# Kernel tuning notes

Measured on AMD Instinct MI355X. Metric: run time of the kernel, lower is better.

## Reference

```python
import jax, jax.numpy as jnp
import numpy as np

N = 50000
E = 800000
IN_C, HID_C, OUT_C = 64, 96, 32


def setup_inputs() -> dict:
    key = jax.random.key(0)
    ks = jax.random.split(key, 8)
    x = jax.random.normal(ks[0], (N, IN_C), dtype=jnp.float32)
    edge_index = jax.random.randint(ks[1], (2, E), 0, N, dtype=jnp.int32)
    W1 = jax.random.normal(ks[2], (IN_C, HID_C), dtype=jnp.float32) / np.sqrt(IN_C)
    b1 = jnp.zeros((HID_C,), jnp.float32)
    W2 = jax.random.normal(ks[3], (HID_C, HID_C), dtype=jnp.float32) / np.sqrt(HID_C)
    b2 = jnp.zeros((HID_C,), jnp.float32)
    Wfc = jax.random.normal(ks[4], (HID_C, OUT_C), dtype=jnp.float32) / np.sqrt(HID_C)
    bfc = jnp.zeros((OUT_C,), jnp.float32)
    return {"x": x, "edge_index": edge_index, "W1": W1, "b1": b1,
            "W2": W2, "b2": b2, "Wfc": Wfc, "bfc": bfc}


def _gcn_conv(x, src, dst, norm, W, b):
    # x' = D^{-1/2}(A+I)D^{-1/2} (x W) + b   (PyG GCNConv default)
    h = x @ W                                # [N, C_out]
    msg = h[src] * norm[:, None]             # gather + edge scaling
    agg = jax.ops.segment_sum(msg, dst, num_segments=N)  # scatter-add
    return agg + b


def reference(x, edge_index, W1, b1, W2, b2, Wfc, bfc):
    loop = jnp.arange(N, dtype=edge_index.dtype)
    src = jnp.concatenate([edge_index[0], loop])  # add self-loops
    dst = jnp.concatenate([edge_index[1], loop])
    deg = jax.ops.segment_sum(jnp.ones(src.shape[0], jnp.float32), dst,
                              num_segments=N)
    dinv = jax.lax.rsqrt(deg)                # deg >= 1 due to self-loops
    norm = dinv[src] * dinv[dst]             # symmetric normalization per edge
    h = jax.nn.relu(_gcn_conv(x, src, dst, norm, W1, b1))
    # dropout omitted (eval mode / identity)
    h = jax.nn.relu(_gcn_conv(h, src, dst, norm, W2, b2))
    return h @ Wfc + bfc
```

## Files before the change

kernel.cpp:

```cpp
#include <hip/hip_runtime.h>
#include <hip/hip_fp16.h>


constexpr int NN = 50000;
constexpr int NE = 800000;
constexpr int NB = 512;
constexpr int NPB = 98;
constexpr int BCAP = 2048;
constexpr int EPB = 4096;
constexpr int P1B = 256;
constexpr int NP1 = (NE + EPB - 1) / EPB;

__global__ void zero_bcnt(int* bcnt) {
  int i = threadIdx.x;
  if (i < NB) bcnt[i] = 0;
}

__global__ __launch_bounds__(P1B) void csr_pass1(const int* __restrict__ ei,
                                                 int* __restrict__ bcnt,
                                                 unsigned* __restrict__ bbuf) {
  __shared__ unsigned sorted[EPB];
  __shared__ int hist[NB];
  __shared__ int lofs[NB];
  __shared__ int cursor[NB];
  __shared__ int gbase[NB];
  __shared__ int psum[P1B];
  const int t = threadIdx.x;
  const int e0 = blockIdx.x * EPB;
  const int ecnt = min(EPB, NE - e0);

  for (int i = t; i < NB; i += P1B) hist[i] = 0;
  __syncthreads();

  for (int i = t; i < ecnt; i += P1B) {
    unsigned dst = (unsigned)ei[NE + e0 + i];
    atomicAdd(&hist[dst / NPB], 1);
  }
  __syncthreads();

  const int h0 = hist[2 * t], h1 = hist[2 * t + 1];
  psum[t] = h0 + h1;
  __syncthreads();
  for (int off = 1; off < P1B; off <<= 1) {
    int v = 0;
    if (t >= off) v = psum[t - off];
    __syncthreads();
    psum[t] += v;
    __syncthreads();
  }
  {
    const int pex = psum[t] - (h0 + h1);
    lofs[2 * t] = pex;
    lofs[2 * t + 1] = pex + h0;
    cursor[2 * t] = pex;
    cursor[2 * t + 1] = pex + h0;
    gbase[2 * t] = atomicAdd(&bcnt[2 * t], h0);
    gbase[2 * t + 1] = atomicAdd(&bcnt[2 * t + 1], h1);
  }
  __syncthreads();

  for (int i = t; i < ecnt; i += P1B) {
    unsigned src = (unsigned)ei[e0 + i];
    unsigned dst = (unsigned)ei[NE + e0 + i];
    unsigned b = dst / NPB;
    unsigned dl = dst - b * NPB;
    int pos = atomicAdd(&cursor[b], 1);
    sorted[pos] = (b << 23) | (dl << 16) | src;
  }
  __syncthreads();

  for (int i = t; i < ecnt; i += P1B) {
    unsigned pw = sorted[i];
    unsigned b = pw >> 23;
    int off_in_b = gbase[b] + (i - lofs[b]);
    if (off_in_b < BCAP)
      bbuf[b * BCAP + off_in_b] = pw & 0x007FFFFFu;
  }
}

__global__ __launch_bounds__(256) void csr_pass2(
    const int* __restrict__ bcnt, const unsigned* __restrict__ bbuf,
    const float* __restrict__ x, int* __restrict__ row_start,
    int* __restrict__ counts, float* __restrict__ dinv,
    __half* __restrict__ u, unsigned short* __restrict__ srcs,
    unsigned* __restrict__ perm) {
  __shared__ int s_red[256];
  __shared__ int s_cnt[128];
  __shared__ int s_scan[128];
  __shared__ int s_cur[128];
  __shared__ float s_dinv[128];
  __shared__ unsigned short s_sorted[BCAP];
  __shared__ int d_hist[64];
  __shared__ int d_cur[64];
  __shared__ int s_permL[NPB];
  const int b = blockIdx.x, t = threadIdx.x;
  const int cnt_b = min(bcnt[b], BCAP);

  int acc = 0;
  for (int j = t; j < b; j += 256) acc += min(bcnt[j], BCAP);
  s_red[t] = acc;
  __syncthreads();
  for (int off = 128; off > 0; off >>= 1) {
    if (t < off) s_red[t] += s_red[t + off];
    __syncthreads();
  }
  const int base = s_red[0];

  if (t < 128) s_cnt[t] = 0;
  __syncthreads();
  for (int i = t; i < cnt_b; i += 256)
    atomicAdd(&s_cnt[bbuf[b * BCAP + i] >> 16], 1);
  __syncthreads();

  if (t < 128) s_scan[t] = s_cnt[t];
  __syncthreads();
  for (int off = 1; off < 128; off <<= 1) {
    int v = 0;
    if (t < 128 && t >= off) v = s_scan[t - off];
    __syncthreads();
    if (t < 128) s_scan[t] += v;
    __syncthreads();
  }
  if (t < 128) s_cur[t] = s_scan[t] - s_cnt[t];

  const int node = b * NPB + t;
  if (t < NPB && node < NN) {
    int c = s_cnt[t];
    row_start[node] = base + s_scan[t] - c;
    counts[node] = c;
    float di = rsqrtf(1.0f + (float)c);
    dinv[node] = di;
    s_dinv[t] = di;
  }
  __syncthreads();

  for (int i = t; i < cnt_b; i += 256) {
    unsigned w = bbuf[b * BCAP + i];
    int pos = atomicAdd(&s_cur[w >> 16], 1);
    s_sorted[pos] = (unsigned short)(w & 0xFFFFu);
  }
  __syncthreads();
  for (int i = t; i < cnt_b; i += 256) srcs[base + i] = s_sorted[i];

  const int na = max(0, min(NN - b * NPB, NPB));
  if (t < 64) d_hist[t] = 0;
  __syncthreads();
  const bool activeN = (t < na);
  const int deg = activeN ? min(s_cnt[t], 63) : 0;
  if (activeN) atomicAdd(&d_hist[deg], 1);
  __syncthreads();
  if (t < 64) d_cur[t] = d_hist[t];
  __syncthreads();
  for (int off = 1; off < 64; off <<= 1) {
    int v = 0;
    if (t < 64 && t >= off) v = d_cur[t - off];
    __syncthreads();
    if (t < 64) d_cur[t] += v;
    __syncthreads();
  }
  if (t < 64) d_cur[t] -= d_hist[t];
  __syncthreads();
  if (activeN) {
    int r = atomicAdd(&d_cur[deg], 1);
    s_permL[r] = t;
  }
  __syncthreads();
  if (t < NPB)
    perm[b * NPB + t] =
        (t < na) ? (unsigned)(b * NPB + s_permL[t]) : 0xFFFFFFFFu;

  const float4* x4 = (const float4*)x;
  for (int i = t; i < NPB * 16; i += 256) {
    int nl = i >> 4, q = i & 15;
    int n = b * NPB + nl;
    if (n < NN) {
      float di = s_dinv[nl];
      float4 v = x4[(size_t)n * 16 + q];
      __half2 h01 = __floats2half2_rn(v.x * di, v.y * di);
      __half2 h23 = __floats2half2_rn(v.z * di, v.w * di);
      uint2 pk;
      pk.x = *(unsigned*)&h01;
      pk.y = *(unsigned*)&h23;
      *(uint2*)(u + (size_t)n * 64 + 4 * q) = pk;
    }
  }
}

__global__ __launch_bounds__(512) void gconv1(
    const unsigned* __restrict__ perm, const int* __restrict__ row_start,
    const int* __restrict__ counts, const unsigned short* __restrict__ srcs,
    const __half* __restrict__ u, const float* __restrict__ W1,
    const float* __restrict__ b1, const float* __restrict__ dinv,
    __half* __restrict__ g1) {
  __shared__ float sh[64 * 65];
  const int t = threadIdx.x;

  {
    const int nl = t >> 3, q = t & 7;
    const unsigned node = perm[blockIdx.x * 64 + nl];
    if (node != 0xFFFFFFFFu) {
      const int n = (int)node;
      const uint4* A4 = (const uint4*)u + q;
      float a[8];
      {
        uint4 v = A4[(size_t)n * 8];
        const __half2* h = (const __half2*)&v;
        #pragma unroll
        for (int k = 0; k < 4; ++k) {
          float2 f = __half22float2(h[k]);
          a[2 * k] = f.x;
          a[2 * k + 1] = f.y;
        }
      }
      const int s0 = row_start[n];
      const int cnt = counts[n];
      int p = 0;
      for (; p + 4 <= cnt; p += 4) {
        int sa = srcs[s0 + p + 0];
        int sb = srcs[s0 + p + 1];
        int sc = srcs[s0 + p + 2];
        int sd = srcs[s0 + p + 3];
        uint4 va = A4[(size_t)sa * 8];
        uint4 vb = A4[(size_t)sb * 8];
        uint4 vc = A4[(size_t)sc * 8];
        uint4 vd = A4[(size_t)sd * 8];
        const __half2* ha = (const __half2*)&va;
        const __half2* hb = (const __half2*)&vb;
        const __half2* hc = (const __half2*)&vc;
        const __half2* hd = (const __half2*)&vd;
        #pragma unroll
        for (int k = 0; k < 4; ++k) {
          float2 fa = __half22float2(ha[k]);
          float2 fb = __half22float2(hb[k]);
          float2 fc = __half22float2(hc[k]);
          float2 fd = __half22float2(hd[k]);
          a[2 * k] += (fa.x + fb.x) + (fc.x + fd.x);
          a[2 * k + 1] += (fa.y + fb.y) + (fc.y + fd.y);
        }
      }
      for (; p < cnt; ++p) {
        uint4 v = A4[(size_t)srcs[s0 + p] * 8];
        const __half2* h = (const __half2*)&v;
        #pragma unroll
        for (int k = 0; k < 4; ++k) {
          float2 f = __half22float2(h[k]);
          a[2 * k] += f.x;
          a[2 * k + 1] += f.y;
        }
      }
      float* sp = sh + nl * 65 + q * 8;
      #pragma unroll
      for (int j = 0; j < 8; ++j) sp[j] = a[j];
    }
  }
  __syncthreads();

  {
    const int nl = t & 63;
    const int c0 = __builtin_amdgcn_readfirstlane((t >> 6) * 12);
    const unsigned node = perm[blockIdx.x * 64 + nl];
    float acc[12] = {};
    const float* __restrict__ hrow = sh + nl * 65;
    #pragma unroll 4
    for (int k = 0; k < 64; ++k) {
      const float hk = hrow[k];
      const float* __restrict__ wrow = W1 + (size_t)k * 96 + c0;
      #pragma unroll
      for (int j = 0; j < 12; ++j) acc[j] = fmaf(hk, wrow[j], acc[j]);
    }
    if (node != 0xFFFFFFFFu) {
      const int n = (int)node;
      const float di = dinv[n];
      __half* op = g1 + (size_t)n * 96 + c0;
      #pragma unroll
      for (int j2 = 0; j2 < 6; ++j2) {
        float r0 = di * fmaxf(fmaf(di, acc[2 * j2 + 0], b1[c0 + 2 * j2 + 0]), 0.f);
        float r1 = di * fmaxf(fmaf(di, acc[2 * j2 + 1], b1[c0 + 2 * j2 + 1]), 0.f);
        __half2 h = __floats2half2_rn(r0, r1);
        *(__half2*)(op + 2 * j2) = h;
      }
    }
  }
}

__global__ __launch_bounds__(768) void gconv2(
    const unsigned* __restrict__ perm, const int* __restrict__ row_start,
    const int* __restrict__ counts, const unsigned short* __restrict__ srcs,
    const __half* __restrict__ g1, const float* __restrict__ W2,
    const float* __restrict__ b2, const float* __restrict__ Wfc,
    const float* __restrict__ bfc, const float* __restrict__ dinv,
    float* __restrict__ out) {
  __shared__ float sh[64 * 97];
  const int t = threadIdx.x;

  {
    const int nl = t / 12, q = t - nl * 12;
    const unsigned node = perm[blockIdx.x * 64 + nl];
    if (node != 0xFFFFFFFFu) {
      const int n = (int)node;
      const uint4* A4 = (const uint4*)g1 + q;
      float a[8];
      {
        uint4 v = A4[(size_t)n * 12];
        const __half2* h = (const __half2*)&v;
        #pragma unroll
        for (int k = 0; k < 4; ++k) {
          float2 f = __half22float2(h[k]);
          a[2 * k] = f.x;
          a[2 * k + 1] = f.y;
        }
      }
      const int s0 = row_start[n];
      const int cnt = counts[n];
      int p = 0;
      for (; p + 4 <= cnt; p += 4) {
        int sa = srcs[s0 + p + 0];
        int sb = srcs[s0 + p + 1];
        int sc = srcs[s0 + p + 2];
        int sd = srcs[s0 + p + 3];
        uint4 va = A4[(size_t)sa * 12];
        uint4 vb = A4[(size_t)sb * 12];
        uint4 vc = A4[(size_t)sc * 12];
        uint4 vd = A4[(size_t)sd * 12];
        const __half2* ha = (const __half2*)&va;
        const __half2* hb = (const __half2*)&vb;
        const __half2* hc = (const __half2*)&vc;
        const __half2* hd = (const __half2*)&vd;
        #pragma unroll
        for (int k = 0; k < 4; ++k) {
          float2 fa = __half22float2(ha[k]);
          float2 fb = __half22float2(hb[k]);
          float2 fc = __half22float2(hc[k]);
          float2 fd = __half22float2(hd[k]);
          a[2 * k] += (fa.x + fb.x) + (fc.x + fd.x);
          a[2 * k + 1] += (fa.y + fb.y) + (fc.y + fd.y);
        }
      }
      for (; p < cnt; ++p) {
        uint4 v = A4[(size_t)srcs[s0 + p] * 12];
        const __half2* h = (const __half2*)&v;
        #pragma unroll
        for (int k = 0; k < 4; ++k) {
          float2 f = __half22float2(h[k]);
          a[2 * k] += f.x;
          a[2 * k + 1] += f.y;
        }
      }
      float* sp = sh + nl * 97 + q * 8;
      #pragma unroll
      for (int j = 0; j < 8; ++j) sp[j] = a[j];
    }
  }
  __syncthreads();

  const int nl = t & 63;
  const unsigned node = perm[blockIdx.x * 64 + nl];
  const int n = (node != 0xFFFFFFFFu) ? (int)node : 0;
  float acc[8] = {};
  {
    const int c0 = __builtin_amdgcn_readfirstlane((t >> 6) * 8);
    const float* __restrict__ hrow = sh + nl * 97;
    #pragma unroll 4
    for (int k = 0; k < 96; ++k) {
      const float hk = hrow[k];
      const float* __restrict__ wrow = W2 + (size_t)k * 96 + c0;
      #pragma unroll
      for (int j = 0; j < 8; ++j) acc[j] = fmaf(hk, wrow[j], acc[j]);
    }
    __syncthreads();
    const float di = dinv[n];
    float* sp = sh + nl * 97 + c0;
    #pragma unroll
    for (int j = 0; j < 8; ++j)
      sp[j] = fmaxf(fmaf(di, acc[j], b2[c0 + j]), 0.f);
  }
  __syncthreads();

  if (t < 512) {
    const int m0 = __builtin_amdgcn_readfirstlane((t >> 6) * 4);
    float o[4] = {};
    const float* __restrict__ hrow = sh + nl * 97;
    #pragma unroll 8
    for (int k = 0; k < 96; ++k) {
      const float hk = hrow[k];
      const float* __restrict__ wr = Wfc + (size_t)k * 32 + m0;
      #pragma unroll
      for (int j = 0; j < 4; ++j) o[j] = fmaf(hk, wr[j], o[j]);
    }
    if (node != 0xFFFFFFFFu) {
      float4 r;
      r.x = o[0] + bfc[m0 + 0];
      r.y = o[1] + bfc[m0 + 1];
      r.z = o[2] + bfc[m0 + 2];
      r.w = o[3] + bfc[m0 + 3];
      *(float4*)(out + (size_t)n * 32 + m0) = r;
    }
  }
}

extern "C" void kernel_launch(void* const* d_in, const int* in_sizes, int n_in,
                              void* d_out, int out_size, void* d_ws,
                              size_t ws_size, hipStream_t stream) {
  const float* x   = (const float*)d_in[0];
  const int*   ei  = (const int*)d_in[1];
  const float* W1  = (const float*)d_in[2];
  const float* b1  = (const float*)d_in[3];
  const float* W2  = (const float*)d_in[4];
  const float* b2  = (const float*)d_in[5];
  const float* Wfc = (const float*)d_in[6];
  const float* bfc = (const float*)d_in[7];
  float* out = (float*)d_out;

  float* dinv = (float*)d_ws;
  float* R0 = dinv + 50048;
  float* R1 = R0 + (size_t)NN * 96;
  int* row_start = (int*)(R1 + (size_t)NN * 96);
  int* counts = row_start + 50048;
  int* bcnt = counts + 50048;
  unsigned short* srcs = (unsigned short*)(bcnt + 512);
  unsigned* perm = (unsigned*)(srcs + NE);
  unsigned* bbuf = (unsigned*)R1;
  __half* u_h = (__half*)R0;
  __half* g1_h = (__half*)R1;

  zero_bcnt<<<1, 512, 0, stream>>>(bcnt);
  csr_pass1<<<NP1, P1B, 0, stream>>>(ei, bcnt, bbuf);
  csr_pass2<<<NB, 256, 0, stream>>>(bcnt, bbuf, x, row_start, counts, dinv,
                                    u_h, srcs, perm);

  constexpr int GB = NB * NPB / 64;

  gconv1<<<GB, 512, 0, stream>>>(perm, row_start, counts, srcs, u_h, W1, b1,
                                 dinv, g1_h);
  gconv2<<<GB, 768, 0, stream>>>(perm, row_start, counts, srcs, g1_h, W2, b2,
                                 Wfc, bfc, dinv, out);
}
```

Measured before the change: 115.8 us.

## Split layer-2 conv into separate gather kernel and fused GEMM+FC kernel

```diff
diff --git a/kernel.cpp b/kernel.cpp
--- a/kernel.cpp
+++ b/kernel.cpp
@@ -283,118 +283,138 @@
   }
 }
 
-__global__ __launch_bounds__(768) void gconv2(
+__global__ __launch_bounds__(256) void gather96(
     const unsigned* __restrict__ perm, const int* __restrict__ row_start,
     const int* __restrict__ counts, const unsigned short* __restrict__ srcs,
-    const __half* __restrict__ g1, const float* __restrict__ W2,
+    const __half* __restrict__ A, __half* __restrict__ B) {
+  constexpr int QP = 12;
+  int gid = blockIdx.x * blockDim.x + threadIdx.x;
+  if (gid >= NB * NPB * QP) return;
+  int i = gid / QP;
+  int q = gid - i * QP;
+  const unsigned node = perm[i];
+  if (node == 0xFFFFFFFFu) return;
+  const int n = (int)node;
+  const uint4* A4 = (const uint4*)A + q;
+
+  float a[8] = {};
+  {
+    uint4 v = A4[(size_t)n * QP];
+    const __half2* h = (const __half2*)&v;
+    #pragma unroll
+    for (int k = 0; k < 4; ++k) {
+      float2 f = __half22float2(h[k]);
+      a[2 * k] = f.x;
+      a[2 * k + 1] = f.y;
+    }
+  }
+  const int s0 = row_start[n];
+  const int cnt = counts[n];
+  int p = 0;
+  for (; p + 4 <= cnt; p += 4) {
+    int sa = srcs[s0 + p + 0];
+    int sb = srcs[s0 + p + 1];
+    int sc = srcs[s0 + p + 2];
+    int sd = srcs[s0 + p + 3];
+    uint4 va = A4[(size_t)sa * QP];
+    uint4 vb = A4[(size_t)sb * QP];
+    uint4 vc = A4[(size_t)sc * QP];
+    uint4 vd = A4[(size_t)sd * QP];
+    const __half2* ha = (const __half2*)&va;
+    const __half2* hb = (const __half2*)&vb;
+    const __half2* hc = (const __half2*)&vc;
+    const __half2* hd = (const __half2*)&vd;
+    #pragma unroll
+    for (int k = 0; k < 4; ++k) {
+      float2 fa = __half22float2(ha[k]);
+      float2 fb = __half22float2(hb[k]);
+      float2 fc = __half22float2(hc[k]);
+      float2 fd = __half22float2(hd[k]);
+      a[2 * k] += (fa.x + fb.x) + (fc.x + fd.x);
+      a[2 * k + 1] += (fa.y + fb.y) + (fc.y + fd.y);
+    }
+  }
+  for (; p < cnt; ++p) {
+    int s = srcs[s0 + p];
+    uint4 v = A4[(size_t)s * QP];
+    const __half2* h = (const __half2*)&v;
+    #pragma unroll
+    for (int k = 0; k < 4; ++k) {
+      float2 f = __half22float2(h[k]);
+      a[2 * k] += f.x;
+      a[2 * k + 1] += f.y;
+    }
+  }
+  __half2 o0 = __floats2half2_rn(a[0], a[1]);
+  __half2 o1 = __floats2half2_rn(a[2], a[3]);
+  __half2 o2 = __floats2half2_rn(a[4], a[5]);
+  __half2 o3 = __floats2half2_rn(a[6], a[7]);
+  uint4 pk;
+  pk.x = *(unsigned*)&o0;
+  pk.y = *(unsigned*)&o1;
+  pk.z = *(unsigned*)&o2;
+  pk.w = *(unsigned*)&o3;
+  *(uint4*)(B + (size_t)n * 96 + 8 * q) = pk;
+}
+
+__global__ __launch_bounds__(256) void sgemm2fc(
+    const __half* __restrict__ X, const float* __restrict__ W2,
     const float* __restrict__ b2, const float* __restrict__ Wfc,
     const float* __restrict__ bfc, const float* __restrict__ dinv,
     float* __restrict__ out) {
-  __shared__ float sh[64 * 97];
+  __shared__ float sh2[64 * 101];
   const int t = threadIdx.x;
-
+  const int nl = t & 63;
+  const int c0 = __builtin_amdgcn_readfirstlane((t >> 6) * 24);
+  const int nr = blockIdx.x * 64 + nl;
+  const bool act = nr < NN;
+  const int n = act ? nr : NN - 1;
+
+  float acc[24] = {};
+  const __half* __restrict__ xh = X + (size_t)n * 96;
+  #pragma unroll 4
+  for (int kq = 0; kq < 24; ++kq) {
+    uint2 xv = *(const uint2*)(xh + 4 * kq);
+    const __half2* hp = (const __half2*)&xv;
+    float2 f01 = __half22float2(hp[0]);
+    float2 f23 = __half22float2(hp[1]);
+    const float xk[4] = {f01.x, f01.y, f23.x, f23.y};
+    #pragma unroll
+    for (int c = 0; c < 4; ++c) {
+      const float* __restrict__ wrow = W2 + (size_t)(4 * kq + c) * 96 + c0;
+      #pragma unroll
+      for (int j = 0; j < 24; ++j)
+        acc[j] = fmaf(xk[c], wrow[j], acc[j]);
+    }
+  }
   {
-    const int nl = t / 12, q = t - nl * 12;
-    const unsigned node = perm[blockIdx.x * 64 + nl];
-    if (node != 0xFFFFFFFFu) {
-      const int n = (int)node;
-      const uint4* A4 = (const uint4*)g1 + q;
-      float a[8];
-      {
-        uint4 v = A4[(size_t)n * 12];
-        const __half2* h = (const __half2*)&v;
-        #pragma unroll
-        for (int k = 0; k < 4; ++k) {
-          float2 f = __half22float2(h[k]);
-          a[2 * k] = f.x;
-          a[2 * k + 1] = f.y;
-        }
-      }
-      const int s0 = row_start[n];
-      const int cnt = counts[n];
-      int p = 0;
-      for (; p + 4 <= cnt; p += 4) {
-        int sa = srcs[s0 + p + 0];
-        int sb = srcs[s0 + p + 1];
-        int sc = srcs[s0 + p + 2];
-        int sd = srcs[s0 + p + 3];
-        uint4 va = A4[(size_t)sa * 12];
-        uint4 vb = A4[(size_t)sb * 12];
-        uint4 vc = A4[(size_t)sc * 12];
-        uint4 vd = A4[(size_t)sd * 12];
-        const __half2* ha = (const __half2*)&va;
-        const __half2* hb = (const __half2*)&vb;
-        const __half2* hc = (const __half2*)&vc;
-        const __half2* hd = (const __half2*)&vd;
-        #pragma unroll
-        for (int k = 0; k < 4; ++k) {
-          float2 fa = __half22float2(ha[k]);
-          float2 fb = __half22float2(hb[k]);
-          float2 fc = __half22float2(hc[k]);
-          float2 fd = __half22float2(hd[k]);
-          a[2 * k] += (fa.x + fb.x) + (fc.x + fd.x);
-          a[2 * k + 1] += (fa.y + fb.y) + (fc.y + fd.y);
-        }
-      }
-      for (; p < cnt; ++p) {
-        uint4 v = A4[(size_t)srcs[s0 + p] * 12];
-        const __half2* h = (const __half2*)&v;
-        #pragma unroll
-        for (int k = 0; k < 4; ++k) {
-          float2 f = __half22float2(h[k]);
-          a[2 * k] += f.x;
-          a[2 * k + 1] += f.y;
-        }
-      }
-      float* sp = sh + nl * 97 + q * 8;
-      #pragma unroll
-      for (int j = 0; j < 8; ++j) sp[j] = a[j];
-    }
-  }
-  __syncthreads();
-
-  const int nl = t & 63;
-  const unsigned node = perm[blockIdx.x * 64 + nl];
-  const int n = (node != 0xFFFFFFFFu) ? (int)node : 0;
-  float acc[8] = {};
-  {
-    const int c0 = __builtin_amdgcn_readfirstlane((t >> 6) * 8);
-    const float* __restrict__ hrow = sh + nl * 97;
-    #pragma unroll 4
-    for (int k = 0; k < 96; ++k) {
-      const float hk = hrow[k];
-      const float* __restrict__ wrow = W2 + (size_t)k * 96 + c0;
-      #pragma unroll
-      for (int j = 0; j < 8; ++j) acc[j] = fmaf(hk, wrow[j], acc[j]);
-    }
-    __syncthreads();
     const float di = dinv[n];
-    float* sp = sh + nl * 97 + c0;
-    #pragma unroll
-    for (int j = 0; j < 8; ++j)
+    float* sp = sh2 + nl * 101 + c0;
+    #pragma unroll
+    for (int j = 0; j < 24; ++j)
       sp[j] = fmaxf(fmaf(di, acc[j], b2[c0 + j]), 0.f);
   }
   __syncthreads();
 
-  if (t < 512) {
-    const int m0 = __builtin_amdgcn_readfirstlane((t >> 6) * 4);
-    float o[4] = {};
-    const float* __restrict__ hrow = sh + nl * 97;
-    #pragma unroll 8
-    for (int k = 0; k < 96; ++k) {
-      const float hk = hrow[k];
-      const float* __restrict__ wr = Wfc + (size_t)k * 32 + m0;
-      #pragma unroll
-      for (int j = 0; j < 4; ++j) o[j] = fmaf(hk, wr[j], o[j]);
-    }
-    if (node != 0xFFFFFFFFu) {
-      float4 r;
-      r.x = o[0] + bfc[m0 + 0];
-      r.y = o[1] + bfc[m0 + 1];
-      r.z = o[2] + bfc[m0 + 2];
-      r.w = o[3] + bfc[m0 + 3];
-      *(float4*)(out + (size_t)n * 32 + m0) = r;
-    }
+  const int m0 = __builtin_amdgcn_readfirstlane((t >> 6) * 8);
+  float o[8] = {};
+  const float* __restrict__ hrow = sh2 + nl * 101;
+  #pragma unroll 8
+  for (int k = 0; k < 96; ++k) {
+    const float hk = hrow[k];
+    const float* __restrict__ wr = Wfc + (size_t)k * 32 + m0;
+    #pragma unroll
+    for (int j = 0; j < 8; ++j) o[j] = fmaf(hk, wr[j], o[j]);
+  }
+  if (act) {
+    float* op = out + (size_t)nr * 32 + m0;
+    float4 r0, r1;
+    r0.x = o[0] + bfc[m0 + 0]; r0.y = o[1] + bfc[m0 + 1];
+    r0.z = o[2] + bfc[m0 + 2]; r0.w = o[3] + bfc[m0 + 3];
+    r1.x = o[4] + bfc[m0 + 4]; r1.y = o[5] + bfc[m0 + 5];
+    r1.z = o[6] + bfc[m0 + 6]; r1.w = o[7] + bfc[m0 + 7];
+    *(float4*)op = r0;
+    *(float4*)(op + 4) = r1;
   }
 }
 
@@ -422,6 +442,7 @@
   unsigned* bbuf = (unsigned*)R1;
   __half* u_h = (__half*)R0;
   __half* g1_h = (__half*)R1;
+  __half* B2h = (__half*)R0;
 
   zero_bcnt<<<1, 512, 0, stream>>>(bcnt);
   csr_pass1<<<NP1, P1B, 0, stream>>>(ei, bcnt, bbuf);
@@ -432,6 +453,8 @@
 
   gconv1<<<GB, 512, 0, stream>>>(perm, row_start, counts, srcs, u_h, W1, b1,
                                  dinv, g1_h);
-  gconv2<<<GB, 768, 0, stream>>>(perm, row_start, counts, srcs, g1_h, W2, b2,
-                                 Wfc, bfc, dinv, out);
-}
+  gather96<<<(NB * NPB * 12 + 255) / 256, 256, 0, stream>>>(
+      perm, row_start, counts, srcs, g1_h, B2h);
+  sgemm2fc<<<(NN + 63) / 64, 256, 0, stream>>>(B2h, W2, b2, Wfc, bfc, dinv,
+                                               out);
+}
```

Result: no change. 116.8 us (+0.8%).
